# Performance work log

Hardware: AMD Instinct MI355X
Metric: run time of the kernel (lower is better)

The kernel has to match this reference:

```python
import jax, jax.numpy as jnp
import numpy as np

E = 768   # embed_dim
N = 12    # num_heads
H = 128   # height
W = 128   # width
D = E // N  # head_dim = 64


def setup_inputs() -> dict:
    key = jax.random.key(0)
    ks = jax.random.split(key, 9)
    s = 0.02
    x = jax.random.normal(ks[0], (1, H * W, E), jnp.float32)
    Wq = jax.random.normal(ks[1], (E, E), jnp.float32) * s
    bq = jnp.zeros((E,), jnp.float32)
    Wk = jax.random.normal(ks[2], (E, E), jnp.float32) * s
    bk = jnp.zeros((E,), jnp.float32)
    Wv = jax.random.normal(ks[3], (E, E), jnp.float32) * s
    bv = jnp.zeros((E,), jnp.float32)
    Wo = jax.random.normal(ks[4], (E, E), jnp.float32) * s
    bo = jnp.zeros((E,), jnp.float32)
    return {"x": x, "Wq": Wq, "bq": bq, "Wk": Wk, "bk": bk,
            "Wv": Wv, "bv": bv, "Wo": Wo, "bo": bo}


def reference(x, Wq, bq, Wk, bk, Wv, bv, Wo, bo):
    # projections (torch Linear: x @ W.T + b)
    q = x @ Wq.T + bq
    k = x @ Wk.T + bk
    v = x @ Wv.T + bv

    # q, k -> (1, N, H, W, D)
    q = q.reshape(1, H, W, N, D).transpose(0, 3, 1, 2, 4)
    k = k.reshape(1, H, W, N, D).transpose(0, 3, 1, 2, 4)

    # --- width-axis attention (per row h) ---
    qr_w = q.transpose(0, 2, 1, 3, 4)  # (1, H, N, W, D)
    kr_w = k.transpose(0, 2, 1, 3, 4)  # (1, H, N, W, D)
    v = v.reshape(1, H, W, N, D).transpose(0, 1, 3, 2, 4)  # (1, H, N, W, D)
    # NOTE: original applies no 1/sqrt(D) scaling
    qk_w = jnp.einsum('bhnwd,bhnvd->bhnwv', qr_w, kr_w)  # (1, H, N, W, W)
    qk_w = jax.nn.softmax(qk_w, axis=-1)
    v = jnp.einsum('bhnwv,bhnvd->bhnwd', qk_w, v)  # (1, H, N, W, D)

    # --- height-axis attention (per column w) ---
    qr_h = q.transpose(0, 3, 1, 2, 4)  # (1, W, N, H, D)
    kr_h = k.transpose(0, 3, 1, 2, 4)  # (1, W, N, H, D)
    v = v.transpose(0, 3, 2, 1, 4)     # (1, W, N, H, D)
    qk_h = jnp.einsum('bwnhd,bwngd->bwnhg', qr_h, kr_h)  # (1, W, N, H, H)
    qk_h = jax.nn.softmax(qk_h, axis=-1)
    out = jnp.einsum('bwnhg,bwngd->bwnhd', qk_h, v)  # (1, W, N, H, D)

    # (1, W, N, H, D) -> (1, H, W, N, D) -> (1, H, W, E)
    out = out.transpose(0, 3, 1, 2, 4).reshape(1, H, W, E)
    out = out @ Wo.T + bo
    return out.reshape(1, H * W, E)
```

## Files before the change

### kernel.cpp

```cpp
#include <hip/hip_runtime.h>

typedef __attribute__((ext_vector_type(4))) float f32x4;
typedef __attribute__((ext_vector_type(8))) unsigned short u16x8;
typedef __attribute__((ext_vector_type(8))) __bf16 bf16x8;

typedef __attribute__((address_space(3))) unsigned lds_u32;
typedef const __attribute__((address_space(1))) unsigned glb_u32;

__device__ __forceinline__ unsigned short f2bf(float f) {
    union { float f; unsigned u; } v; v.f = f;
    unsigned r = v.u + 0x7fffu + ((v.u >> 16) & 1u);
    return (unsigned short)(r >> 16);
}

__device__ __forceinline__ f32x4 mfma16(u16x8 a, u16x8 b, f32x4 c) {
    return __builtin_amdgcn_mfma_f32_16x16x32_bf16(
        __builtin_bit_cast(bf16x8, a), __builtin_bit_cast(bf16x8, b), c, 0, 0, 0);
}

__device__ __forceinline__ void gload16(const unsigned short* g, unsigned short* l) {
    __builtin_amdgcn_global_load_lds((glb_u32*)g, (lds_u32*)l, 16, 0, 0);
}

__global__ void cvt_f32_bf16(const float* __restrict__ src,
                             unsigned short* __restrict__ dst, int n) {
    int stride = gridDim.x * blockDim.x * 4;
    for (int i = (blockIdx.x * blockDim.x + threadIdx.x) * 4; i < n; i += stride) {
        float4 f = *reinterpret_cast<const float4*>(src + i);
        ushort4 o;
        o.x = f2bf(f.x); o.y = f2bf(f.y); o.z = f2bf(f.z); o.w = f2bf(f.w);
        *reinterpret_cast<ushort4*>(dst + i) = o;
    }
}

template<bool OUTF32>
__global__ __launch_bounds__(256) void gemm_bt(
    const unsigned short* __restrict__ A,
    const unsigned short* __restrict__ B,
    const float* __restrict__ b0, const float* __restrict__ b1, const float* __restrict__ b2,
    void* __restrict__ C0, void* __restrict__ C1, void* __restrict__ C2,
    int K)
{
    __shared__ unsigned short As[128 * 32];
    __shared__ unsigned short Bs[128 * 32];
    const int t = threadIdx.x, lane = t & 63, wave = t >> 6;
    const int wm = wave >> 1, wn = wave & 1;
    const long m0 = (long)blockIdx.x * 128;
    const long n0 = (long)blockIdx.y * 128;

    const unsigned short* Ag = A + (m0 + wave * 32 + (lane >> 2)) * K + (lane & 3) * 8;
    const unsigned short* Bg = B + (n0 + wave * 32 + (lane >> 2)) * K + (lane & 3) * 8;
    unsigned short* AsW = &As[wave * 1024];
    unsigned short* BsW = &Bs[wave * 1024];

    f32x4 acc[4][4] = {};

    for (int k0 = 0; k0 < K; k0 += 32) {
        __syncthreads();
        gload16(Ag + k0,          AsW);
        gload16(Ag + 16 * K + k0, AsW + 512);
        gload16(Bg + k0,          BsW);
        gload16(Bg + 16 * K + k0, BsW + 512);
        __syncthreads();
        u16x8 af[4], bfr[4];
        #pragma unroll
        for (int i = 0; i < 4; ++i)
            af[i]  = *(const u16x8*)&As[(wm * 64 + i * 16 + (lane & 15)) * 32 + (lane >> 4) * 8];
        #pragma unroll
        for (int i = 0; i < 4; ++i)
            bfr[i] = *(const u16x8*)&Bs[(wn * 64 + i * 16 + (lane & 15)) * 32 + (lane >> 4) * 8];
        #pragma unroll
        for (int mi = 0; mi < 4; ++mi)
            #pragma unroll
            for (int ni = 0; ni < 4; ++ni)
                acc[mi][ni] = mfma16(af[mi], bfr[ni], acc[mi][ni]);
    }

    #pragma unroll
    for (int mi = 0; mi < 4; ++mi) {
        #pragma unroll
        for (int ni = 0; ni < 4; ++ni) {
            int coln = (int)n0 + wn * 64 + ni * 16 + (lane & 15);
            int which = coln / 768;
            int nl = coln - which * 768;
            const float* bs = which == 0 ? b0 : (which == 1 ? b1 : b2);
            void* Cp       = which == 0 ? C0 : (which == 1 ? C1 : C2);
            float bias = bs[nl];
            #pragma unroll
            for (int q = 0; q < 4; ++q) {
                long row = m0 + wm * 64 + mi * 16 + ((lane >> 4) << 2) + q;
                float val = acc[mi][ni][q] + bias;
                if (OUTF32) ((float*)Cp)[row * 768 + nl] = val;
                else ((unsigned short*)Cp)[row * 768 + nl] = f2bf(val);
            }
        }
    }
}

__global__ __launch_bounds__(256, 3) void attn128(
    const unsigned short* __restrict__ Q,
    const unsigned short* __restrict__ K,
    const unsigned short* __restrict__ V,
    unsigned short* __restrict__ O,
    int mult, int stride)
{
    __shared__ unsigned short QK[2][128][72];
    __shared__ unsigned short Vst[64][136];
    unsigned short (*Qs)[72] = QK[0];
    unsigned short (*Ks)[72] = QK[1];
    unsigned short (*Ps)[136] = (unsigned short (*)[136])&QK[0][0][0];

    const int pos = blockIdx.x, head = blockIdx.y;
    const int t = threadIdx.x, wave = t >> 6, lane = t & 63;

    for (int p = 0; p < 4; ++p) {
        int f = p * 2048 + t * 8;
        int r = f >> 6;
        int d = f & 63;
        long g = ((long)(pos * mult + r * stride)) * 768 + head * 64 + d;
        *(u16x8*)&Qs[r][d] = *(const u16x8*)&Q[g];
        *(u16x8*)&Ks[r][d] = *(const u16x8*)&K[g];
        u16x8 vv = *(const u16x8*)&V[g];
        #pragma unroll
        for (int j = 0; j < 8; ++j) Vst[d + j][r] = vv[j];
    }
    __syncthreads();

    const int rb = wave * 32;
    f32x4 s[2][8] = {};
    #pragma unroll
    for (int d0 = 0; d0 < 64; d0 += 32) {
        u16x8 a[2], b[8];
        #pragma unroll
        for (int mi = 0; mi < 2; ++mi)
            a[mi] = *(const u16x8*)&Qs[rb + mi * 16 + (lane & 15)][d0 + (lane >> 4) * 8];
        #pragma unroll
        for (int ni = 0; ni < 8; ++ni)
            b[ni] = *(const u16x8*)&Ks[ni * 16 + (lane & 15)][d0 + (lane >> 4) * 8];
        #pragma unroll
        for (int mi = 0; mi < 2; ++mi)
            #pragma unroll
            for (int ni = 0; ni < 8; ++ni)
                s[mi][ni] = mfma16(a[mi], b[ni], s[mi][ni]);
    }
    __syncthreads();

    #pragma unroll
    for (int mi = 0; mi < 2; ++mi) {
        #pragma unroll
        for (int q = 0; q < 4; ++q) {
            float m = -1e30f;
            #pragma unroll
            for (int ni = 0; ni < 8; ++ni) m = fmaxf(m, s[mi][ni][q]);
            m = fmaxf(m, __shfl_xor(m, 1));
            m = fmaxf(m, __shfl_xor(m, 2));
            m = fmaxf(m, __shfl_xor(m, 4));
            m = fmaxf(m, __shfl_xor(m, 8));
            float p[8], sum = 0.f;
            #pragma unroll
            for (int ni = 0; ni < 8; ++ni) { p[ni] = __expf(s[mi][ni][q] - m); sum += p[ni]; }
            sum += __shfl_xor(sum, 1);
            sum += __shfl_xor(sum, 2);
            sum += __shfl_xor(sum, 4);
            sum += __shfl_xor(sum, 8);
            float inv = 1.0f / sum;
            int row = rb + mi * 16 + ((lane >> 4) << 2) + q;
            #pragma unroll
            for (int ni = 0; ni < 8; ++ni)
                Ps[row][ni * 16 + (lane & 15)] = f2bf(p[ni] * inv);
        }
    }
    __syncthreads();

    f32x4 o[2][4] = {};
    #pragma unroll
    for (int v0 = 0; v0 < 128; v0 += 32) {
        u16x8 a[2], b[4];
        #pragma unroll
        for (int mi = 0; mi < 2; ++mi)
            a[mi] = *(const u16x8*)&Ps[rb + mi * 16 + (lane & 15)][v0 + (lane >> 4) * 8];
        #pragma unroll
        for (int ni = 0; ni < 4; ++ni)
            b[ni] = *(const u16x8*)&Vst[ni * 16 + (lane & 15)][v0 + (lane >> 4) * 8];
        #pragma unroll
        for (int mi = 0; mi < 2; ++mi)
            #pragma unroll
            for (int ni = 0; ni < 4; ++ni)
                o[mi][ni] = mfma16(a[mi], b[ni], o[mi][ni]);
    }

    #pragma unroll
    for (int mi = 0; mi < 2; ++mi)
        #pragma unroll
        for (int ni = 0; ni < 4; ++ni)
            #pragma unroll
            for (int q = 0; q < 4; ++q) {
                int row = rb + mi * 16 + ((lane >> 4) << 2) + q;
                int col = ni * 16 + (lane & 15);
                long g = ((long)(pos * mult + row * stride)) * 768 + head * 64 + col;
                O[g] = f2bf(o[mi][ni][q]);
            }
}

extern "C" void kernel_launch(void* const* d_in, const int* in_sizes, int n_in,
                              void* d_out, int out_size, void* d_ws, size_t ws_size,
                              hipStream_t stream) {
    const float* x  = (const float*)d_in[0];
    const float* Wq = (const float*)d_in[1];
    const float* bq = (const float*)d_in[2];
    const float* Wk = (const float*)d_in[3];
    const float* bk = (const float*)d_in[4];
    const float* Wv = (const float*)d_in[5];
    const float* bv = (const float*)d_in[6];
    const float* Wo = (const float*)d_in[7];
    const float* bo = (const float*)d_in[8];
    float* out = (float*)d_out;

    const size_t MS = (size_t)16384 * 768;
    const size_t WS = (size_t)768 * 768;
    unsigned short* xb   = (unsigned short*)d_ws;
    unsigned short* Qb   = xb + MS;
    unsigned short* Kb   = Qb + MS;
    unsigned short* Vb   = Kb + MS;
    unsigned short* Wqkv = Vb + MS;
    unsigned short* Wob  = Wqkv + 3 * WS;

    cvt_f32_bf16<<<2048, 256, 0, stream>>>(x,  xb, (int)MS);
    cvt_f32_bf16<<<576, 256, 0, stream>>>(Wq, Wqkv,           (int)WS);
    cvt_f32_bf16<<<576, 256, 0, stream>>>(Wk, Wqkv + WS,      (int)WS);
    cvt_f32_bf16<<<576, 256, 0, stream>>>(Wv, Wqkv + 2 * WS,  (int)WS);
    cvt_f32_bf16<<<576, 256, 0, stream>>>(Wo, Wob,            (int)WS);

    gemm_bt<false><<<dim3(128, 18), 256, 0, stream>>>(
        xb, Wqkv, bq, bk, bv, Qb, Kb, Vb, 768);

    attn128<<<dim3(128, 12), 256, 0, stream>>>(Qb, Kb, Vb, xb, 128, 1);
    attn128<<<dim3(128, 12), 256, 0, stream>>>(Qb, Kb, xb, Vb, 1, 128);

    gemm_bt<true><<<dim3(128, 6), 256, 0, stream>>>(
        Vb, Wob, bo, bo, bo, out, out, out, 768);
}
```

Before: 192.7 us.

## Replace GEMMs with 256x256 double-buffered swizzled-LDS pipelined kernel and merge weight conversions

Replaces the 128x128 single-buffered GEMM with a 256x256 tile, 8-wave kernel. It uses a 128 KB double-buffered LDS with an XOR swizzle, explicit vmcnt/lgkmcnt waits, interleaved loads and MFMA phases with setprio, and block-index swizzling for L2 locality. The four weight conversion launches are merged into one kernel. This aims to raise MFMA utilization and hide global load latency, at the cost of a much more fragile hand-scheduled pipeline. The output-projection GEMM now launches only 192 blocks, which may underfill the GPU.

```diff
diff --git a/kernel.cpp b/kernel.cpp
--- a/kernel.cpp
+++ b/kernel.cpp
@@ -21,6 +21,13 @@
 __device__ __forceinline__ void gload16(const unsigned short* g, unsigned short* l) {
     __builtin_amdgcn_global_load_lds((glb_u32*)g, (lds_u32*)l, 16, 0, 0);
 }
+
+#define CFENCE() asm volatile("" ::: "memory")
+#define SCHED0() __builtin_amdgcn_sched_barrier(0)
+#define BARF() do { CFENCE(); __builtin_amdgcn_s_barrier(); CFENCE(); } while (0)
+#define WAITLGKM0() do { asm volatile("s_waitcnt lgkmcnt(0)" ::: "memory"); SCHED0(); } while (0)
+#define WAITVM6()   do { asm volatile("s_waitcnt vmcnt(6)" ::: "memory"); SCHED0(); } while (0)
+#define WAITVM0()   do { asm volatile("s_waitcnt vmcnt(0)" ::: "memory"); SCHED0(); } while (0)
 
 __global__ void cvt_f32_bf16(const float* __restrict__ src,
                              unsigned short* __restrict__ dst, int n) {
@@ -33,68 +40,155 @@
     }
 }
 
+__global__ void cvt4_f32_bf16(const float* __restrict__ s0, const float* __restrict__ s1,
+                              const float* __restrict__ s2, const float* __restrict__ s3,
+                              unsigned short* __restrict__ dst, int per) {
+    int total = per * 4;
+    int stride = gridDim.x * blockDim.x * 4;
+    for (int i = (blockIdx.x * blockDim.x + threadIdx.x) * 4; i < total; i += stride) {
+        int w = i / per, off = i - w * per;
+        const float* s = w == 0 ? s0 : w == 1 ? s1 : w == 2 ? s2 : s3;
+        float4 f = *reinterpret_cast<const float4*>(s + off);
+        ushort4 o;
+        o.x = f2bf(f.x); o.y = f2bf(f.y); o.z = f2bf(f.z); o.w = f2bf(f.w);
+        *reinterpret_cast<ushort4*>(dst + i) = o;
+    }
+}
+
 template<bool OUTF32>
-__global__ __launch_bounds__(256) void gemm_bt(
+__global__ __launch_bounds__(512, 2) void gemm256(
     const unsigned short* __restrict__ A,
     const unsigned short* __restrict__ B,
     const float* __restrict__ b0, const float* __restrict__ b1, const float* __restrict__ b2,
     void* __restrict__ C0, void* __restrict__ C1, void* __restrict__ C2,
-    int K)
+    int K, int NBY)
 {
-    __shared__ unsigned short As[128 * 32];
-    __shared__ unsigned short Bs[128 * 32];
+    __shared__ char lds[131072];
     const int t = threadIdx.x, lane = t & 63, wave = t >> 6;
-    const int wm = wave >> 1, wn = wave & 1;
-    const long m0 = (long)blockIdx.x * 128;
-    const long n0 = (long)blockIdx.y * 128;
-
-    const unsigned short* Ag = A + (m0 + wave * 32 + (lane >> 2)) * K + (lane & 3) * 8;
-    const unsigned short* Bg = B + (n0 + wave * 32 + (lane >> 2)) * K + (lane & 3) * 8;
-    unsigned short* AsW = &As[wave * 1024];
-    unsigned short* BsW = &Bs[wave * 1024];
-
-    f32x4 acc[4][4] = {};
-
-    for (int k0 = 0; k0 < K; k0 += 32) {
-        __syncthreads();
-        gload16(Ag + k0,          AsW);
-        gload16(Ag + 16 * K + k0, AsW + 512);
-        gload16(Bg + k0,          BsW);
-        gload16(Bg + 16 * K + k0, BsW + 512);
-        __syncthreads();
-        u16x8 af[4], bfr[4];
-        #pragma unroll
-        for (int i = 0; i < 4; ++i)
-            af[i]  = *(const u16x8*)&As[(wm * 64 + i * 16 + (lane & 15)) * 32 + (lane >> 4) * 8];
-        #pragma unroll
-        for (int i = 0; i < 4; ++i)
-            bfr[i] = *(const u16x8*)&Bs[(wn * 64 + i * 16 + (lane & 15)) * 32 + (lane >> 4) * 8];
+    const int wm = wave >> 2, wn = wave & 3;
+
+    const int nwg = gridDim.x;
+    const int bid = blockIdx.x;
+    const int swzb = (bid & 7) * (nwg >> 3) + (bid >> 3);
+    const long m0 = (long)(swzb / NBY) * 256;
+    const long n0 = (long)(swzb % NBY) * 256;
+
+    const int NT = K >> 6;
+
+    const int rloc = t >> 3;
+    const int cel  = ((t & 7) ^ ((t >> 3) & 7)) << 3;
+    const unsigned short* Abase = A + (m0 + rloc) * (long)K + cel;
+    const unsigned short* Bbase = B + (n0 + rloc) * (long)K + cel;
+
+    auto STAGEA = [&](int kt, int h) {
+        char* dst = lds + ((kt & 1) << 15) + (h << 14) + (wave << 10);
+        const unsigned short* src = Abase + (long)(h * 128) * K + kt * 64;
+        gload16(src, (unsigned short*)dst);
+        gload16(src + (long)64 * K, (unsigned short*)(dst + 8192));
+    };
+    auto STAGEB = [&](int kt, int h) {
+        char* dst = lds + 65536 + ((kt & 1) << 15) + (h << 14) + (wave << 10);
+        const unsigned short* src = Bbase + (long)(h * 128) * K + kt * 64;
+        gload16(src, (unsigned short*)dst);
+        gload16(src + (long)64 * K, (unsigned short*)(dst + 8192));
+    };
+
+    f32x4 acc[8][4] = {};
+    u16x8 a[4][2], bl0[2][2], bl1[2][2];
+
+    auto LDA8 = [&](int slot, int mh) {
+        const char* buf = lds + (slot << 15) + (wm << 14);
         #pragma unroll
         for (int mi = 0; mi < 4; ++mi)
             #pragma unroll
-            for (int ni = 0; ni < 4; ++ni)
-                acc[mi][ni] = mfma16(af[mi], bfr[ni], acc[mi][ni]);
-    }
-
-    #pragma unroll
-    for (int mi = 0; mi < 4; ++mi) {
-        #pragma unroll
-        for (int ni = 0; ni < 4; ++ni) {
-            int coln = (int)n0 + wn * 64 + ni * 16 + (lane & 15);
-            int which = coln / 768;
-            int nl = coln - which * 768;
-            const float* bs = which == 0 ? b0 : (which == 1 ? b1 : b2);
-            void* Cp       = which == 0 ? C0 : (which == 1 ? C1 : C2);
-            float bias = bs[nl];
-            #pragma unroll
-            for (int q = 0; q < 4; ++q) {
-                long row = m0 + wm * 64 + mi * 16 + ((lane >> 4) << 2) + q;
-                float val = acc[mi][ni][q] + bias;
-                if (OUTF32) ((float*)Cp)[row * 768 + nl] = val;
-                else ((unsigned short*)Cp)[row * 768 + nl] = f2bf(val);
+            for (int kk = 0; kk < 2; ++kk) {
+                int r = mh * 64 + mi * 16 + (lane & 15);
+                int cb = kk * 64 + (lane >> 4) * 16;
+                a[mi][kk] = *(const u16x8*)(buf + r * 128 + (cb ^ ((r & 7) << 4)));
             }
-        }
-    }
+    };
+    auto LDB4 = [&](int slot, int nh, u16x8 bf[2][2]) {
+        const char* buf = lds + 65536 + (slot << 15) + ((wn >> 1) << 14);
+        #pragma unroll
+        for (int ni = 0; ni < 2; ++ni)
+            #pragma unroll
+            for (int kk = 0; kk < 2; ++kk) {
+                int r = (wn & 1) * 64 + nh * 32 + ni * 16 + (lane & 15);
+                int cb = kk * 64 + (lane >> 4) * 16;
+                bf[ni][kk] = *(const u16x8*)(buf + r * 128 + (cb ^ ((r & 7) << 4)));
+            }
+    };
+    auto MF16 = [&](int mh, int nh, u16x8 bf[2][2]) {
+        __builtin_amdgcn_s_setprio(1);
+        #pragma unroll
+        for (int mi = 0; mi < 4; ++mi)
+            #pragma unroll
+            for (int ni = 0; ni < 2; ++ni)
+                #pragma unroll
+                for (int kk = 0; kk < 2; ++kk)
+                    acc[mh * 4 + mi][nh * 2 + ni] =
+                        mfma16(a[mi][kk], bf[ni][kk], acc[mh * 4 + mi][nh * 2 + ni]);
+        __builtin_amdgcn_s_setprio(0);
+    };
+
+    STAGEA(0, 0); CFENCE(); STAGEB(0, 0); CFENCE(); STAGEB(0, 1); CFENCE();
+    STAGEA(0, 1); CFENCE();
+    STAGEA(1, 0); CFENCE(); STAGEB(1, 0); CFENCE(); STAGEB(1, 1); CFENCE();
+    SCHED0();
+    WAITVM0();
+    BARF();
+
+    for (int I = 0; I < (NT >> 1); ++I) {
+        const int tb = 2 * I + 1;
+        int t2 = 2 * I + 2; if (t2 >= NT) t2 -= 2;
+        int t3 = 2 * I + 3; if (t3 >= NT) t3 -= 2;
+
+        LDA8(0, 0); LDB4(0, 0, bl0); STAGEA(tb, 1);
+        SCHED0(); BARF(); WAITLGKM0();
+        MF16(0, 0, bl0); BARF();
+        LDB4(0, 1, bl1);
+        SCHED0(); BARF(); WAITLGKM0();
+        MF16(0, 1, bl1); BARF();
+        LDA8(0, 1); STAGEB(t2, 0);
+        SCHED0(); BARF(); WAITLGKM0();
+        MF16(1, 1, bl1); BARF();
+        STAGEA(t2, 0); STAGEB(t2, 1);
+        SCHED0(); WAITVM6(); BARF();
+        MF16(1, 0, bl0); BARF();
+        LDA8(1, 0); LDB4(1, 0, bl0); STAGEA(t2, 1);
+        SCHED0(); BARF(); WAITLGKM0();
+        MF16(0, 0, bl0); BARF();
+        LDB4(1, 1, bl1);
+        SCHED0(); BARF(); WAITLGKM0();
+        MF16(0, 1, bl1); BARF();
+        LDA8(1, 1); STAGEB(t3, 0);
+        SCHED0(); BARF(); WAITLGKM0();
+        MF16(1, 1, bl1); BARF();
+        STAGEA(t3, 0); STAGEB(t3, 1);
+        SCHED0(); WAITVM6(); BARF();
+        MF16(1, 0, bl0); BARF();
+    }
+
+    #pragma unroll
+    for (int mh = 0; mh < 2; ++mh)
+        #pragma unroll
+        for (int mi = 0; mi < 4; ++mi)
+            #pragma unroll
+            for (int nf = 0; nf < 4; ++nf) {
+                int coln = (int)n0 + wn * 64 + nf * 16 + (lane & 15);
+                int which = coln / 768;
+                int nl = coln - which * 768;
+                const float* bs = which == 0 ? b0 : (which == 1 ? b1 : b2);
+                void* Cp       = which == 0 ? C0 : (which == 1 ? C1 : C2);
+                float bias = bs[nl];
+                #pragma unroll
+                for (int q = 0; q < 4; ++q) {
+                    long row = m0 + wm * 128 + mh * 64 + mi * 16 + ((lane >> 4) << 2) + q;
+                    float val = acc[mh * 4 + mi][nf][q] + bias;
+                    if (OUTF32) ((float*)Cp)[row * 768 + nl] = val;
+                    else ((unsigned short*)Cp)[row * 768 + nl] = f2bf(val);
+                }
+            }
 }
 
 __global__ __launch_bounds__(256, 3) void attn128(
@@ -225,18 +319,15 @@
     unsigned short* Wqkv = Vb + MS;
     unsigned short* Wob  = Wqkv + 3 * WS;
 
-    cvt_f32_bf16<<<2048, 256, 0, stream>>>(x,  xb, (int)MS);
-    cvt_f32_bf16<<<576, 256, 0, stream>>>(Wq, Wqkv,           (int)WS);
-    cvt_f32_bf16<<<576, 256, 0, stream>>>(Wk, Wqkv + WS,      (int)WS);
-    cvt_f32_bf16<<<576, 256, 0, stream>>>(Wv, Wqkv + 2 * WS,  (int)WS);
-    cvt_f32_bf16<<<576, 256, 0, stream>>>(Wo, Wob,            (int)WS);
-
-    gemm_bt<false><<<dim3(128, 18), 256, 0, stream>>>(
-        xb, Wqkv, bq, bk, bv, Qb, Kb, Vb, 768);
+    cvt_f32_bf16<<<2048, 256, 0, stream>>>(x, xb, (int)MS);
+    cvt4_f32_bf16<<<2304, 256, 0, stream>>>(Wq, Wk, Wv, Wo, Wqkv, (int)WS);
+
+    gemm256<false><<<576, 512, 0, stream>>>(
+        xb, Wqkv, bq, bk, bv, Qb, Kb, Vb, 768, 9);
 
     attn128<<<dim3(128, 12), 256, 0, stream>>>(Qb, Kb, Vb, xb, 128, 1);
     attn128<<<dim3(128, 12), 256, 0, stream>>>(Qb, Kb, xb, Vb, 1, 128);
 
-    gemm_bt<true><<<dim3(128, 6), 256, 0, stream>>>(
-        Vb, Wob, bo, bo, bo, out, out, out, 768);
-}
+    gemm256<true><<<192, 512, 0, stream>>>(
+        Vb, Wob, bo, bo, bo, out, out, out, 768, 3);
+}
```

Result: faster. 184.1 us (-4.4%).

## Double-buffer GEMM K-tiles with swizzled LDS and XCD-aware block remap

Applied to the files above, without the earlier changes.

The GEMM now stages 64-wide K tiles into two LDS buffers using direct global-to-LDS loads. The next tile is prefetched while the current one runs through MFMA, and there is one barrier per tile instead of two. The LDS layout gets an XOR swizzle to avoid bank conflicts, and the 1D grid is remapped so consecutive blocks group across the 8 XCDs for L2 reuse. The four weight conversions are merged into one launch. In exchange the GEMM uses 64KB of LDS and relies on hand-written waitcnt/barrier asm, and the last iteration reloads a dummy tile.

```diff
diff --git a/kernel.cpp b/kernel.cpp
--- a/kernel.cpp
+++ b/kernel.cpp
@@ -21,6 +21,9 @@
 __device__ __forceinline__ void gload16(const unsigned short* g, unsigned short* l) {
     __builtin_amdgcn_global_load_lds((glb_u32*)g, (lds_u32*)l, 16, 0, 0);
 }
+
+#define BARM() asm volatile("s_barrier" ::: "memory")
+#define WAITVM0() asm volatile("s_waitcnt vmcnt(0)" ::: "memory")
 
 __global__ void cvt_f32_bf16(const float* __restrict__ src,
                              unsigned short* __restrict__ dst, int n) {
@@ -33,54 +36,101 @@
     }
 }
 
+__global__ void cvt4_f32_bf16(const float* __restrict__ s0, const float* __restrict__ s1,
+                              const float* __restrict__ s2, const float* __restrict__ s3,
+                              unsigned short* __restrict__ dst, int per) {
+    int total = per * 4;
+    int stride = gridDim.x * blockDim.x * 4;
+    for (int i = (blockIdx.x * blockDim.x + threadIdx.x) * 4; i < total; i += stride) {
+        int w = i / per, off = i - w * per;
+        const float* s = w == 0 ? s0 : w == 1 ? s1 : w == 2 ? s2 : s3;
+        float4 f = *reinterpret_cast<const float4*>(s + off);
+        ushort4 o;
+        o.x = f2bf(f.x); o.y = f2bf(f.y); o.z = f2bf(f.z); o.w = f2bf(f.w);
+        *reinterpret_cast<ushort4*>(dst + i) = o;
+    }
+}
+
 template<bool OUTF32>
-__global__ __launch_bounds__(256) void gemm_bt(
+__global__ __launch_bounds__(256, 2) void gemm128(
     const unsigned short* __restrict__ A,
     const unsigned short* __restrict__ B,
     const float* __restrict__ b0, const float* __restrict__ b1, const float* __restrict__ b2,
     void* __restrict__ C0, void* __restrict__ C1, void* __restrict__ C2,
-    int K)
+    int K, int NBY)
 {
-    __shared__ unsigned short As[128 * 32];
-    __shared__ unsigned short Bs[128 * 32];
+    __shared__ char lds[65536];
     const int t = threadIdx.x, lane = t & 63, wave = t >> 6;
     const int wm = wave >> 1, wn = wave & 1;
-    const long m0 = (long)blockIdx.x * 128;
-    const long n0 = (long)blockIdx.y * 128;
-
-    const unsigned short* Ag = A + (m0 + wave * 32 + (lane >> 2)) * K + (lane & 3) * 8;
-    const unsigned short* Bg = B + (n0 + wave * 32 + (lane >> 2)) * K + (lane & 3) * 8;
-    unsigned short* AsW = &As[wave * 1024];
-    unsigned short* BsW = &Bs[wave * 1024];
+
+    const int nwg = gridDim.x;
+    const int bid = blockIdx.x;
+    const int swzb = (bid & 7) * (nwg >> 3) + (bid >> 3);
+    const long m0 = (long)(swzb / NBY) * 128;
+    const long n0 = (long)(swzb % NBY) * 128;
+
+    const int NT = K >> 6;
+
+    const int rloc = t >> 3;
+    const int cel  = ((t & 7) ^ ((t >> 3) & 7)) << 3;
+    const unsigned short* Ab = A + (m0 + rloc) * (long)K + cel;
+    const unsigned short* Bb = B + (n0 + rloc) * (long)K + cel;
+
+    auto STAGE = [&](int kt) {
+        char* da = lds + ((kt & 1) << 14) + (wave << 10);
+        char* db = lds + 32768 + ((kt & 1) << 14) + (wave << 10);
+        const unsigned short* sa = Ab + kt * 64;
+        const unsigned short* sb = Bb + kt * 64;
+        #pragma unroll
+        for (int j = 0; j < 4; ++j) {
+            gload16(sa + (long)(j * 32) * K, (unsigned short*)(da + j * 4096));
+            gload16(sb + (long)(j * 32) * K, (unsigned short*)(db + j * 4096));
+        }
+    };
 
     f32x4 acc[4][4] = {};
-
-    for (int k0 = 0; k0 < K; k0 += 32) {
-        __syncthreads();
-        gload16(Ag + k0,          AsW);
-        gload16(Ag + 16 * K + k0, AsW + 512);
-        gload16(Bg + k0,          BsW);
-        gload16(Bg + 16 * K + k0, BsW + 512);
-        __syncthreads();
-        u16x8 af[4], bfr[4];
-        #pragma unroll
-        for (int i = 0; i < 4; ++i)
-            af[i]  = *(const u16x8*)&As[(wm * 64 + i * 16 + (lane & 15)) * 32 + (lane >> 4) * 8];
-        #pragma unroll
-        for (int i = 0; i < 4; ++i)
-            bfr[i] = *(const u16x8*)&Bs[(wn * 64 + i * 16 + (lane & 15)) * 32 + (lane >> 4) * 8];
-        #pragma unroll
-        for (int mi = 0; mi < 4; ++mi)
-            #pragma unroll
-            for (int ni = 0; ni < 4; ++ni)
-                acc[mi][ni] = mfma16(af[mi], bfr[ni], acc[mi][ni]);
-    }
-
-    #pragma unroll
-    for (int mi = 0; mi < 4; ++mi) {
-        #pragma unroll
-        for (int ni = 0; ni < 4; ++ni) {
-            int coln = (int)n0 + wn * 64 + ni * 16 + (lane & 15);
+    u16x8 af[4][2], bf[4][2];
+
+    auto LD = [&](int slot) {
+        const char* bufA = lds + (slot << 14);
+        const char* bufB = lds + 32768 + (slot << 14);
+        #pragma unroll
+        for (int f = 0; f < 4; ++f)
+            #pragma unroll
+            for (int kk = 0; kk < 2; ++kk) {
+                int ra = wm * 64 + f * 16 + (lane & 15);
+                int rb = wn * 64 + f * 16 + (lane & 15);
+                int cb = kk * 64 + (lane >> 4) * 16;
+                af[f][kk] = *(const u16x8*)(bufA + ra * 128 + (cb ^ ((ra & 7) << 4)));
+                bf[f][kk] = *(const u16x8*)(bufB + rb * 128 + (cb ^ ((rb & 7) << 4)));
+            }
+    };
+
+    STAGE(0);
+    WAITVM0();
+    BARM();
+
+    for (int kt = 0; kt < NT; ++kt) {
+        int nx = kt + 1;
+        if (nx >= NT) nx = NT - 2;
+        STAGE(nx);
+        LD(kt & 1);
+        #pragma unroll
+        for (int kk = 0; kk < 2; ++kk)
+            #pragma unroll
+            for (int mi = 0; mi < 4; ++mi)
+                #pragma unroll
+                for (int nf = 0; nf < 4; ++nf)
+                    acc[mi][nf] = mfma16(af[mi][kk], bf[nf][kk], acc[mi][nf]);
+        WAITVM0();
+        BARM();
+    }
+
+    #pragma unroll
+    for (int mi = 0; mi < 4; ++mi)
+        #pragma unroll
+        for (int nf = 0; nf < 4; ++nf) {
+            int coln = (int)n0 + wn * 64 + nf * 16 + (lane & 15);
             int which = coln / 768;
             int nl = coln - which * 768;
             const float* bs = which == 0 ? b0 : (which == 1 ? b1 : b2);
@@ -89,12 +139,11 @@
             #pragma unroll
             for (int q = 0; q < 4; ++q) {
                 long row = m0 + wm * 64 + mi * 16 + ((lane >> 4) << 2) + q;
-                float val = acc[mi][ni][q] + bias;
+                float val = acc[mi][nf][q] + bias;
                 if (OUTF32) ((float*)Cp)[row * 768 + nl] = val;
                 else ((unsigned short*)Cp)[row * 768 + nl] = f2bf(val);
             }
         }
-    }
 }
 
 __global__ __launch_bounds__(256, 3) void attn128(
@@ -225,18 +274,15 @@
     unsigned short* Wqkv = Vb + MS;
     unsigned short* Wob  = Wqkv + 3 * WS;
 
-    cvt_f32_bf16<<<2048, 256, 0, stream>>>(x,  xb, (int)MS);
-    cvt_f32_bf16<<<576, 256, 0, stream>>>(Wq, Wqkv,           (int)WS);
-    cvt_f32_bf16<<<576, 256, 0, stream>>>(Wk, Wqkv + WS,      (int)WS);
-    cvt_f32_bf16<<<576, 256, 0, stream>>>(Wv, Wqkv + 2 * WS,  (int)WS);
-    cvt_f32_bf16<<<576, 256, 0, stream>>>(Wo, Wob,            (int)WS);
-
-    gemm_bt<false><<<dim3(128, 18), 256, 0, stream>>>(
-        xb, Wqkv, bq, bk, bv, Qb, Kb, Vb, 768);
+    cvt_f32_bf16<<<2048, 256, 0, stream>>>(x, xb, (int)MS);
+    cvt4_f32_bf16<<<2304, 256, 0, stream>>>(Wq, Wk, Wv, Wo, Wqkv, (int)WS);
+
+    gemm128<false><<<2304, 256, 0, stream>>>(
+        xb, Wqkv, bq, bk, bv, Qb, Kb, Vb, 768, 18);
 
     attn128<<<dim3(128, 12), 256, 0, stream>>>(Qb, Kb, Vb, xb, 128, 1);
     attn128<<<dim3(128, 12), 256, 0, stream>>>(Qb, Kb, xb, Vb, 1, 128);
 
-    gemm_bt<true><<<dim3(128, 6), 256, 0, stream>>>(
-        Vb, Wob, bo, bo, bo, out, out, out, 768);
-}
+    gemm128<true><<<768, 256, 0, stream>>>(
+        Vb, Wob, bo, bo, bo, out, out, out, 768, 6);
+}
```

Result: faster. 182.3 us (-5.4%).
